# Kernel tuning notes

Measured on AMD Instinct MI355X. Metric: run time of the kernel, lower is better.

The kernel has to match this reference:

```python
import jax, jax.numpy as jnp
import numpy as np

B, N, D = 4, 4096, 256
HEADS, OUT = 4, 64


def setup_inputs() -> dict:
    key = jax.random.key(0)
    ks = jax.random.split(key, 6)
    features = jax.random.normal(ks[0], (B, N, D), dtype=jnp.float32)
    adj = jax.random.randint(ks[1], (B, N, N), 0, 2).astype(jnp.float32)
    s_fc = 1.0 / np.sqrt(D)
    W_fc = jax.random.uniform(ks[2], (OUT * HEADS, D), jnp.float32, -s_fc, s_fc)
    b_fc = jnp.zeros((OUT * HEADS,), jnp.float32)
    s_a = 1.0 / np.sqrt(2 * OUT * HEADS)
    W_attn = jax.random.uniform(ks[3], (HEADS, 2 * OUT * HEADS), jnp.float32, -s_a, s_a)
    b_attn = jax.random.uniform(ks[4], (HEADS,), jnp.float32, -s_a, s_a)
    return {"features": features, "adj": adj, "W_fc": W_fc, "b_fc": b_fc,
            "W_attn": W_attn, "b_attn": b_attn}


def reference(features, adj, W_fc, b_fc, W_attn, b_attn):
    b, n, d = features.shape
    heads = W_attn.shape[0]
    out = W_fc.shape[0] // heads
    # h: [b, n, heads, out]  (fc output reshaped head-major, matching torch .view)
    h = (features @ W_fc.T + b_fc).reshape(b, n, heads, out)
    # attn linear on concat([h_src, h_dst]) flattened as (heads, [src_out | dst_out]),
    # then mean over the `heads` output dim -> score decomposes additively:
    # e[b,i,j] = src[b,j] + dst[b,i] + mean(b_attn)
    Wa = W_attn.reshape(heads, heads, 2 * out)  # [k_out, h_in, 2*out]
    W_src = Wa[:, :, :out].mean(axis=0)   # [heads, out]
    W_dst = Wa[:, :, out:].mean(axis=0)   # [heads, out]
    src = jnp.einsum('bjho,ho->bj', h, W_src)  # depends on source node j
    dst = jnp.einsum('biho,ho->bi', h, W_dst)  # depends on dest node i
    scores = dst[:, :, None] + src[:, None, :] + b_attn.mean()  # [b, n, n]
    scores = scores + (1.0 - adj) * (-1e9)
    alpha = jax.nn.softmax(scores, axis=2)  # softmax over source nodes j
    # torch einsum 'bijk,bjkl->bijl' broadcasts attn's size-1 k against heads,
    # so aggregation uses sum over heads of h; final .mean(dim=2) divides by n.
    h_sum = h.sum(axis=2)  # [b, n, out]
    out_feat = jnp.einsum('bij,bjl->bil', alpha, h_sum) / n
    return out_feat
```

## Files before the change

### kernel.cpp

```cpp
#include <hip/hip_runtime.h>
#include <stdint.h>
#include <math.h>


#define Bz   4
#define Nn   4096
#define Dd   256
#define OUTd 64
#define GTR  80
#define BKf  128
#define NTt  (Nn / BKf)

typedef float    f32x4   __attribute__((ext_vector_type(4)));
typedef __fp16   fp16x2  __attribute__((ext_vector_type(2)));
typedef _Float16 half8_t __attribute__((ext_vector_type(8)));

__device__ inline half8_t cvt8(float4 a, float4 b) {
  union { fp16x2 h2[4]; half8_t h8; } r;
  r.h2[0] = __builtin_amdgcn_cvt_pkrtz(a.x, a.y);
  r.h2[1] = __builtin_amdgcn_cvt_pkrtz(a.z, a.w);
  r.h2[2] = __builtin_amdgcn_cvt_pkrtz(b.x, b.y);
  r.h2[3] = __builtin_amdgcn_cvt_pkrtz(b.z, b.w);
  return r.h8;
}

__device__ inline void gload_lds16(const float* g, float* l) {
  __builtin_amdgcn_global_load_lds((const __attribute__((address_space(1))) void*)g,
                                   (__attribute__((address_space(3))) void*)l, 16, 0, 0);
}

__global__ __launch_bounds__(256) void k_prep(const float* __restrict__ W_fc,
                                              const float* __restrict__ W_attn,
                                              const float* __restrict__ b_fc,
                                              _Float16* __restrict__ Ut,
                                              float* __restrict__ hb,
                                              float* __restrict__ sb) {
  const int bx = blockIdx.x, t = threadIdx.x;
  if (bx < 64) {
    const int l = bx, d = t;
    float v = W_fc[l * 256 + d] + W_fc[(64 + l) * 256 + d] +
              W_fc[(128 + l) * 256 + d] + W_fc[(192 + l) * 256 + d];
    Ut[l * 256 + d] = (_Float16)v;
    return;
  }
  __shared__ float ws_sh[256];
  {
    const int h = t >> 6, o = t & 63;
    float s = 0.f;
    for (int k = 0; k < 4; ++k) s += W_attn[k * 512 + h * 128 + o];
    ws_sh[t] = s * 0.25f;
  }
  __syncthreads();
  if (bx == 64) {
    const int d = t;
    float v = 0.f;
    for (int ho = 0; ho < 256; ++ho) v += W_fc[ho * 256 + d] * ws_sh[ho];
    Ut[64 * 256 + d] = (_Float16)v;
  } else {
    __shared__ float red[256];
    red[t] = b_fc[t] * ws_sh[t];
    if (t < 64) hb[t] = b_fc[t] + b_fc[64 + t] + b_fc[128 + t] + b_fc[192 + t];
    __syncthreads();
    if (t == 0) {
      float a = 0.f;
      for (int i = 0; i < 256; ++i) a += red[i];
      *sb = a;
    }
  }
}

__global__ __launch_bounds__(256) void k_feat(const float* __restrict__ feat,
                                              const _Float16* __restrict__ Ut,
                                              const float* __restrict__ hb,
                                              const float* __restrict__ sb,
                                              _Float16* __restrict__ Gt) {
  const int b = blockIdx.y;
  const int tid = threadIdx.x;
  const int lane = tid & 63;
  const int wv = tid >> 6;
  const int ln15 = lane & 15;
  const int quad = lane >> 4;
  const int j = blockIdx.x * 64 + wv * 16 + ln15;

  const float* frow = feat + ((size_t)b * Nn + j) * Dd + quad * 8;
  f32x4 acc0 = {0,0,0,0}, acc1 = {0,0,0,0}, acc2 = {0,0,0,0}, acc3 = {0,0,0,0}, acc4 = {0,0,0,0};

  #pragma unroll
  for (int d0 = 0; d0 < Dd; d0 += 32) {
    float4 F0 = *(const float4*)(frow + d0);
    float4 F1 = *(const float4*)(frow + d0 + 4);
    half8_t bf = cvt8(F0, F1);
    const _Float16* up = Ut + (size_t)ln15 * Dd + d0 + quad * 8;
    acc0 = __builtin_amdgcn_mfma_f32_16x16x32_f16(*(const half8_t*)(up + 0 * 16 * Dd), bf, acc0, 0, 0, 0);
    acc1 = __builtin_amdgcn_mfma_f32_16x16x32_f16(*(const half8_t*)(up + 1 * 16 * Dd), bf, acc1, 0, 0, 0);
    acc2 = __builtin_amdgcn_mfma_f32_16x16x32_f16(*(const half8_t*)(up + 2 * 16 * Dd), bf, acc2, 0, 0, 0);
    acc3 = __builtin_amdgcn_mfma_f32_16x16x32_f16(*(const half8_t*)(up + 3 * 16 * Dd), bf, acc3, 0, 0, 0);
    acc4 = __builtin_amdgcn_mfma_f32_16x16x32_f16(*(const half8_t*)(up + 4 * 16 * Dd), bf, acc4, 0, 0, 0);
  }
  float srcv = __shfl(acc4[0], ln15) + sb[0];
  float p = expf(srcv);
  _Float16* gb = Gt + (size_t)b * GTR * Nn;
  #pragma unroll
  for (int r = 0; r < 4; ++r) {
    int lb = quad * 4 + r;
    gb[(size_t)(0  + lb) * Nn + j] = (_Float16)((acc0[r] + hb[0  + lb]) * p);
    gb[(size_t)(16 + lb) * Nn + j] = (_Float16)((acc1[r] + hb[16 + lb]) * p);
    gb[(size_t)(32 + lb) * Nn + j] = (_Float16)((acc2[r] + hb[32 + lb]) * p);
    gb[(size_t)(48 + lb) * Nn + j] = (_Float16)((acc3[r] + hb[48 + lb]) * p);
  }
  if (quad == 0) gb[(size_t)64 * Nn + j] = (_Float16)p;
}

__global__ __launch_bounds__(256) void k_agg(const float* __restrict__ adj,
                                             const _Float16* __restrict__ Gt,
                                             float* __restrict__ out) {
  __shared__ float lds[16384];
  const int b = blockIdx.y;
  const int tid = threadIdx.x;
  const int lane = tid & 63;
  const int wv = tid >> 6;
  const int ln15 = lane & 15;
  const int quad = lane >> 4;
  const int i0 = blockIdx.x * 64 + wv * 16;

  const float* gstage = adj + ((size_t)b * Nn + (i0 + (lane >> 5))) * (size_t)Nn + (lane & 31) * 4;
  float* ldsw = &lds[wv * 4096];

  const _Float16* g0 = Gt + ((size_t)b * GTR + ln15) * Nn + quad * 8;
  const _Float16* g1 = g0 + (size_t)16 * Nn;
  const _Float16* g2 = g0 + (size_t)32 * Nn;
  const _Float16* g3 = g0 + (size_t)48 * Nn;
  const _Float16* g4 = g0 + (size_t)64 * Nn;

  f32x4 acc0 = {0,0,0,0}, acc1 = {0,0,0,0}, acc2 = {0,0,0,0}, acc3 = {0,0,0,0}, acc4 = {0,0,0,0};

  #pragma unroll
  for (int m = 0; m < 8; ++m)
    gload_lds16(gstage + (size_t)(m * 2) * Nn, ldsw + m * 256);

  for (int t = 0; t < NTt; ++t) {
    const int k0 = t * BKf;
    const int cb = t & 1;
    const int nb = cb ^ 1;

    half8_t bg0[4], bg1[4], bg2[4], bg3[4], bg4[4];
    #pragma unroll
    for (int s = 0; s < 4; ++s) {
      const int kk = k0 + s * 32;
      bg0[s] = *(const half8_t*)(g0 + kk);
      bg1[s] = *(const half8_t*)(g1 + kk);
      bg2[s] = *(const half8_t*)(g2 + kk);
      bg3[s] = *(const half8_t*)(g3 + kk);
      bg4[s] = *(const half8_t*)(g4 + kk);
    }
    __builtin_amdgcn_sched_barrier(0);

    const int kn = (t + 1 < NTt) ? (t + 1) * BKf : 0;
    #pragma unroll
    for (int m = 0; m < 8; ++m)
      gload_lds16(gstage + (size_t)(m * 2) * Nn + kn, ldsw + nb * 2048 + m * 256);

    asm volatile("s_waitcnt vmcnt(28)" ::: "memory");

    const float* lb = ldsw + cb * 2048 + ln15 * 128;
    #pragma unroll
    for (int s = 0; s < 4; ++s) {
      float4 A0 = *(const float4*)(lb + s * 32 + quad * 8);
      float4 A1 = *(const float4*)(lb + s * 32 + quad * 8 + 4);
      half8_t aF = cvt8(A0, A1);
      acc0 = __builtin_amdgcn_mfma_f32_16x16x32_f16(aF, bg0[s], acc0, 0, 0, 0);
      acc1 = __builtin_amdgcn_mfma_f32_16x16x32_f16(aF, bg1[s], acc1, 0, 0, 0);
      acc2 = __builtin_amdgcn_mfma_f32_16x16x32_f16(aF, bg2[s], acc2, 0, 0, 0);
      acc3 = __builtin_amdgcn_mfma_f32_16x16x32_f16(aF, bg3[s], acc3, 0, 0, 0);
      acc4 = __builtin_amdgcn_mfma_f32_16x16x32_f16(aF, bg4[s], acc4, 0, 0, 0);
    }
  }

  float den0 = __shfl(acc4[0], lane & 48);
  float den1 = __shfl(acc4[1], lane & 48);
  float den2 = __shfl(acc4[2], lane & 48);
  float den3 = __shfl(acc4[3], lane & 48);
  const float invn = 1.0f / (float)Nn;
  float* orow = out + ((size_t)b * Nn + i0) * OUTd;
  #pragma unroll
  for (int r = 0; r < 4; ++r) {
    float d = (r == 0) ? den0 : (r == 1) ? den1 : (r == 2) ? den2 : den3;
    float rd = invn / d;
    int ir = quad * 4 + r;
    orow[(size_t)ir * OUTd + 0  + ln15] = acc0[r] * rd;
    orow[(size_t)ir * OUTd + 16 + ln15] = acc1[r] * rd;
    orow[(size_t)ir * OUTd + 32 + ln15] = acc2[r] * rd;
    orow[(size_t)ir * OUTd + 48 + ln15] = acc3[r] * rd;
  }
}

extern "C" void kernel_launch(void* const* d_in, const int* in_sizes, int n_in,
                              void* d_out, int out_size, void* d_ws, size_t ws_size,
                              hipStream_t stream) {
  const float* feat   = (const float*)d_in[0];
  const float* adj    = (const float*)d_in[1];
  const float* W_fc   = (const float*)d_in[2];
  const float* b_fc   = (const float*)d_in[3];
  const float* W_attn = (const float*)d_in[4];
  (void)d_in[5];
  float* out = (float*)d_out;

  char* ws = (char*)d_ws;
  _Float16* Gt = (_Float16*)ws;
  _Float16* Ut = (_Float16*)(ws + 2621440);
  float*    hb  = (float*)(ws + 2621440 + 40960);
  float*    sb  = (float*)(ws + 2621440 + 40960 + 256);

  k_prep<<<66, 256, 0, stream>>>(W_fc, W_attn, b_fc, Ut, hb, sb);
  k_feat<<<dim3(64, 4), 256, 0, stream>>>(feat, Ut, hb, sb, Gt);
  k_agg<<<dim3(64, 4), 256, 0, stream>>>(adj, Gt, out);
}
```

Baseline: 411.7 us.

## Pack adjacency into bitmasks in a wide pre-pass and expand bits in aggregation

A new set of blocks is added to the feature kernel's launch. They stream the float adjacency matrix with wave ballots and pack it into one bit per entry. The aggregation kernel then reads the compact bitmask instead of staging float adjacency through LDS, and expands each byte into fp16 0/1 MFMA operands. The aim is to read the large adjacency matrix with far more parallelism than the 256-block aggregation grid allowed, and to shrink the aggregation kernel's own memory traffic. The cost is an extra 8 MB write and read, and per-lane bit-expansion ALU work inside the MFMA loop.

```diff
diff --git a/kernel.cpp b/kernel.cpp
--- a/kernel.cpp
+++ b/kernel.cpp
@@ -8,8 +8,7 @@
 #define Dd   256
 #define OUTd 64
 #define GTR  80
-#define BKf  128
-#define NTt  (Nn / BKf)
+#define NT   32
 
 typedef float    f32x4   __attribute__((ext_vector_type(4)));
 typedef __fp16   fp16x2  __attribute__((ext_vector_type(2)));
@@ -24,9 +23,12 @@
   return r.h8;
 }
 
-__device__ inline void gload_lds16(const float* g, float* l) {
-  __builtin_amdgcn_global_load_lds((const __attribute__((address_space(1))) void*)g,
-                                   (__attribute__((address_space(3))) void*)l, 16, 0, 0);
+__device__ inline half8_t expand8(unsigned int byte) {
+  half8_t e;
+  #pragma unroll
+  for (int r = 0; r < 8; ++r)
+    e[r] = (_Float16)(float)((byte >> r) & 1u);
+  return e;
 }
 
 __global__ __launch_bounds__(256) void k_prep(const float* __restrict__ W_fc,
@@ -69,18 +71,41 @@
   }
 }
 
-__global__ __launch_bounds__(256) void k_feat(const float* __restrict__ feat,
-                                              const _Float16* __restrict__ Ut,
-                                              const float* __restrict__ hb,
-                                              const float* __restrict__ sb,
-                                              _Float16* __restrict__ Gt) {
-  const int b = blockIdx.y;
+__global__ __launch_bounds__(256) void k_featpack(const float* __restrict__ feat,
+                                                  const float* __restrict__ adj,
+                                                  const _Float16* __restrict__ Ut,
+                                                  const float* __restrict__ hb,
+                                                  const float* __restrict__ sb,
+                                                  _Float16* __restrict__ Gt,
+                                                  unsigned long long* __restrict__ Pk) {
+  const int bx = blockIdx.x;
   const int tid = threadIdx.x;
   const int lane = tid & 63;
   const int wv = tid >> 6;
+
+  if (bx >= 256) {
+    const int gw = (bx - 256) * 4 + wv;
+    #pragma unroll 1
+    for (int rr = 0; rr < 4; ++rr) {
+      const size_t row = (size_t)gw * 4 + rr;
+      const float* arow = adj + row * (size_t)Nn + lane;
+      unsigned long long myw = 0ull;
+      #pragma unroll 4
+      for (int wi = 0; wi < 64; ++wi) {
+        float v = arow[(size_t)wi * 64];
+        unsigned long long bal = __ballot(v != 0.0f);
+        if (lane == wi) myw = bal;
+      }
+      Pk[row * 64 + lane] = myw;
+    }
+    return;
+  }
+
+  const int b = bx >> 6;
+  const int jblk = bx & 63;
   const int ln15 = lane & 15;
   const int quad = lane >> 4;
-  const int j = blockIdx.x * 64 + wv * 16 + ln15;
+  const int j = jblk * 64 + wv * 16 + ln15;
 
   const float* frow = feat + ((size_t)b * Nn + j) * Dd + quad * 8;
   f32x4 acc0 = {0,0,0,0}, acc1 = {0,0,0,0}, acc2 = {0,0,0,0}, acc3 = {0,0,0,0}, acc4 = {0,0,0,0};
@@ -111,10 +136,9 @@
   if (quad == 0) gb[(size_t)64 * Nn + j] = (_Float16)p;
 }
 
-__global__ __launch_bounds__(256) void k_agg(const float* __restrict__ adj,
+__global__ __launch_bounds__(256) void k_agg(const uint4* __restrict__ Pk,
                                              const _Float16* __restrict__ Gt,
                                              float* __restrict__ out) {
-  __shared__ float lds[16384];
   const int b = blockIdx.y;
   const int tid = threadIdx.x;
   const int lane = tid & 63;
@@ -123,8 +147,7 @@
   const int quad = lane >> 4;
   const int i0 = blockIdx.x * 64 + wv * 16;
 
-  const float* gstage = adj + ((size_t)b * Nn + (i0 + (lane >> 5))) * (size_t)Nn + (lane & 31) * 4;
-  float* ldsw = &lds[wv * 4096];
+  const uint4* prow = Pk + ((size_t)b * Nn + i0 + ln15) * 32;
 
   const _Float16* g0 = Gt + ((size_t)b * GTR + ln15) * Nn + quad * 8;
   const _Float16* g1 = g0 + (size_t)16 * Nn;
@@ -134,15 +157,10 @@
 
   f32x4 acc0 = {0,0,0,0}, acc1 = {0,0,0,0}, acc2 = {0,0,0,0}, acc3 = {0,0,0,0}, acc4 = {0,0,0,0};
 
-  #pragma unroll
-  for (int m = 0; m < 8; ++m)
-    gload_lds16(gstage + (size_t)(m * 2) * Nn, ldsw + m * 256);
-
-  for (int t = 0; t < NTt; ++t) {
-    const int k0 = t * BKf;
-    const int cb = t & 1;
-    const int nb = cb ^ 1;
-
+  #pragma unroll 2
+  for (int t = 0; t < NT; ++t) {
+    const int k0 = t * 128;
+    uint4 w4 = prow[t];
     half8_t bg0[4], bg1[4], bg2[4], bg3[4], bg4[4];
     #pragma unroll
     for (int s = 0; s < 4; ++s) {
@@ -153,21 +171,10 @@
       bg3[s] = *(const half8_t*)(g3 + kk);
       bg4[s] = *(const half8_t*)(g4 + kk);
     }
-    __builtin_amdgcn_sched_barrier(0);
-
-    const int kn = (t + 1 < NTt) ? (t + 1) * BKf : 0;
-    #pragma unroll
-    for (int m = 0; m < 8; ++m)
-      gload_lds16(gstage + (size_t)(m * 2) * Nn + kn, ldsw + nb * 2048 + m * 256);
-
-    asm volatile("s_waitcnt vmcnt(28)" ::: "memory");
-
-    const float* lb = ldsw + cb * 2048 + ln15 * 128;
     #pragma unroll
     for (int s = 0; s < 4; ++s) {
-      float4 A0 = *(const float4*)(lb + s * 32 + quad * 8);
-      float4 A1 = *(const float4*)(lb + s * 32 + quad * 8 + 4);
-      half8_t aF = cvt8(A0, A1);
+      const unsigned int word = (s == 0) ? w4.x : (s == 1) ? w4.y : (s == 2) ? w4.z : w4.w;
+      half8_t aF = expand8((word >> (quad * 8)) & 0xffu);
       acc0 = __builtin_amdgcn_mfma_f32_16x16x32_f16(aF, bg0[s], acc0, 0, 0, 0);
       acc1 = __builtin_amdgcn_mfma_f32_16x16x32_f16(aF, bg1[s], acc1, 0, 0, 0);
       acc2 = __builtin_amdgcn_mfma_f32_16x16x32_f16(aF, bg2[s], acc2, 0, 0, 0);
@@ -210,8 +217,9 @@
   _Float16* Ut = (_Float16*)(ws + 2621440);
   float*    hb  = (float*)(ws + 2621440 + 40960);
   float*    sb  = (float*)(ws + 2621440 + 40960 + 256);
+  unsigned long long* Pk = (unsigned long long*)(ws + 4194304);
 
   k_prep<<<66, 256, 0, stream>>>(W_fc, W_attn, b_fc, Ut, hb, sb);
-  k_feat<<<dim3(64, 4), 256, 0, stream>>>(feat, Ut, hb, sb, Gt);
-  k_agg<<<dim3(64, 4), 256, 0, stream>>>(adj, Gt, out);
-}
+  k_featpack<<<1280, 256, 0, stream>>>(feat, adj, Ut, hb, sb, Gt, Pk);
+  k_agg<<<dim3(64, 4), 256, 0, stream>>>((const uint4*)Pk, Gt, out);
+}
```

Result: slower. 473.6 us (+15.1%).
